# Optimization experiments

Hardware: AMD Instinct MI355X
Metric: run time of the kernel (lower is better)

The kernel has to match this reference:

```python
import jax, jax.numpy as jnp
import numpy as np
import math

K_DIM = 1024
HEADS = 16

def setup_inputs() -> dict:
    key = jax.random.key(0)
    ks = jax.random.split(key, 6)
    b, N, k = 4, 2048, K_DIM
    sc = 1.0 / math.sqrt(k)
    return {
        "x": jax.random.normal(ks[0], (b, N, k), dtype=jnp.float32),
        "Wk": jax.random.normal(ks[1], (k, k), dtype=jnp.float32) * sc,
        "Wq": jax.random.normal(ks[2], (k, k), dtype=jnp.float32) * sc,
        "Wv": jax.random.normal(ks[3], (k, k), dtype=jnp.float32) * sc,
        "Wu": jax.random.normal(ks[4], (k, k), dtype=jnp.float32) * sc,
        "bu": jax.random.normal(ks[5], (k,), dtype=jnp.float32) * 0.01,
    }

def reference(x, Wk, Wq, Wv, Wu, bu):
    b, N, k = x.shape
    h = HEADS
    s = k // h
    # torch Linear: y = x @ W^T
    Q = (x @ Wq.T).reshape(b, N, h, s).transpose(0, 2, 1, 3)  # [b,h,N,s]
    Kh = (x @ Wk.T).reshape(b, N, h, s).transpose(0, 2, 1, 3)
    V = (x @ Wv.T).reshape(b, N, h, s).transpose(0, 2, 1, 3)
    scores = jnp.einsum('bhid,bhjd->bhij', Q, Kh) / math.sqrt(s)  # [b,h,N,N]
    attn = jax.nn.softmax(scores, axis=-1)
    out = jnp.einsum('bhij,bhjd->bhid', attn, V)  # [b,h,N,s]
    out = out.transpose(0, 2, 1, 3).reshape(b, N, k)
    return out @ Wu.T + bu
```

## Files before the change

### kernel.cpp

```cpp
#include <hip/hip_runtime.h>

typedef __bf16 bf16;
typedef __bf16 bf16x4 __attribute__((ext_vector_type(4)));
typedef __bf16 bf16x8 __attribute__((ext_vector_type(8)));
typedef float  f32x4  __attribute__((ext_vector_type(4)));

#define MFMA16(a, b, c) __builtin_amdgcn_mfma_f32_16x16x32_bf16((a), (b), (c), 0, 0, 0)

__device__ __forceinline__ void async_copy16(const void* g, void* l) {
  __builtin_amdgcn_global_load_lds(
      (const __attribute__((address_space(1))) unsigned int*)g,
      (__attribute__((address_space(3))) unsigned int*)l, 16, 0, 0);
}

struct CvtArgs {
  const float* src[5];
  bf16* dst[5];
  int blk_start[6];
};
__global__ void k_cvt_all(CvtArgs a) {
  int b = blockIdx.x;
  int seg = 0;
#pragma unroll
  for (int s = 1; s < 5; ++s) seg += (b >= a.blk_start[s]);
  int i = (b - a.blk_start[seg]) * 2048 + threadIdx.x * 8;
  float4 v0 = *(const float4*)(a.src[seg] + i);
  float4 v1 = *(const float4*)(a.src[seg] + i + 4);
  bf16x8 o = { (bf16)v0.x, (bf16)v0.y, (bf16)v0.z, (bf16)v0.w,
               (bf16)v1.x, (bf16)v1.y, (bf16)v1.z, (bf16)v1.w };
  *(bf16x8*)(a.dst[seg] + i) = o;
}

template <int OUTF32>
__device__ __forceinline__ void gemm128_body(
    const bf16* __restrict__ A, const bf16* __restrict__ B, void* __restrict__ Cp,
    const float* __restrict__ bias, int m0, int n0, int N, int K) {
  __shared__ alignas(16) bf16 As[2][128 * 32];
  __shared__ alignas(16) bf16 Bs[2][128 * 32];
  const int tid = threadIdx.x;
  const int lane = tid & 63;
  const int w = tid >> 6;
  const int quad = lane >> 4;
  const int l16 = lane & 15;
  const int wr = (w >> 1) * 64;
  const int wc = (w & 1) * 64;

  const int srow = tid >> 2;
  const int skk = (tid & 3) * 8;
  const bf16* Ag = A + (long)(m0 + srow) * K + skk;
  const bf16* Bg = B + (long)(n0 + srow) * K + skk;
  const long half = 64L * K;
  bf16* AsW0 = As[0] + w * 512;
  bf16* BsW0 = Bs[0] + w * 512;
  bf16* AsW1 = As[1] + w * 512;
  bf16* BsW1 = Bs[1] + w * 512;

  f32x4 acc[4][4];
#pragma unroll
  for (int i = 0; i < 4; ++i)
#pragma unroll
    for (int j = 0; j < 4; ++j) acc[i][j] = (f32x4){0.f, 0.f, 0.f, 0.f};

  for (int k0 = 0; k0 < K; k0 += 64) {
    async_copy16(Ag + k0, AsW0);
    async_copy16(Ag + half + k0, AsW0 + 2048);
    async_copy16(Bg + k0, BsW0);
    async_copy16(Bg + half + k0, BsW0 + 2048);
    async_copy16(Ag + k0 + 32, AsW1);
    async_copy16(Ag + half + k0 + 32, AsW1 + 2048);
    async_copy16(Bg + k0 + 32, BsW1);
    async_copy16(Bg + half + k0 + 32, BsW1 + 2048);
    __syncthreads();
#pragma unroll
    for (int p = 0; p < 2; ++p) {
      const bf16* AsP = As[p];
      const bf16* BsP = Bs[p];
      bf16x8 af[4], bfr[4];
#pragma unroll
      for (int i = 0; i < 4; ++i)
        af[i] = *(const bf16x8*)&AsP[(wr + i * 16 + l16) * 32 + quad * 8];
#pragma unroll
      for (int j = 0; j < 4; ++j)
        bfr[j] = *(const bf16x8*)&BsP[(wc + j * 16 + l16) * 32 + quad * 8];
#pragma unroll
      for (int i = 0; i < 4; ++i)
#pragma unroll
        for (int j = 0; j < 4; ++j) acc[i][j] = MFMA16(af[i], bfr[j], acc[i][j]);
    }
    __syncthreads();
  }

#pragma unroll
  for (int i = 0; i < 4; ++i)
#pragma unroll
    for (int j = 0; j < 4; ++j)
#pragma unroll
      for (int r = 0; r < 4; ++r) {
        long row = m0 + wr + i * 16 + quad * 4 + r;
        int col = n0 + wc + j * 16 + l16;
        if (OUTF32)
          ((float*)Cp)[row * N + col] = acc[i][j][r] + bias[col];
        else
          ((bf16*)Cp)[row * N + col] = (bf16)acc[i][j][r];
      }
}

#define VMCNT(n) asm volatile("s_waitcnt vmcnt(" #n ")" ::: "memory")
#define SBAR()   asm volatile("s_barrier" ::: "memory")

__device__ __forceinline__ void rdA8(bf16x8 a[4][2], const bf16* S, int base, int c0) {
#pragma unroll
  for (int f = 0; f < 4; ++f) {
    a[f][0] = *(const bf16x8*)(S + base + f * 2048 + c0);
    a[f][1] = *(const bf16x8*)(S + base + f * 2048 + (c0 ^ 32));
  }
}
__device__ __forceinline__ void rdB4(bf16x8 b[2][2], const bf16* S, int base, int c0) {
#pragma unroll
  for (int f = 0; f < 2; ++f) {
    b[f][0] = *(const bf16x8*)(S + base + f * 4096 + c0);
    b[f][1] = *(const bf16x8*)(S + base + f * 4096 + (c0 ^ 32));
  }
}
__device__ __forceinline__ void stg(const bf16* g, bf16* d) {
  async_copy16(g, d);
  async_copy16(g + 64 * 1024, d + 4096);
}

#define MQ(qa, qb)                                             \
  do {                                                         \
    __builtin_amdgcn_s_setprio(1);                             \
    _Pragma("unroll") for (int fa = 0; fa < 4; ++fa)           \
      _Pragma("unroll") for (int fb = 0; fb < 2; ++fb) {       \
        f32x4& cc = acc[(qa) * 4 + fa][(qb) * 2 + fb];         \
        cc = MFMA16(a[fa][0], b[fb][0], cc);                   \
        cc = MFMA16(a[fa][1], b[fb][1], cc);                   \
      }                                                        \
    __builtin_amdgcn_s_setprio(0);                             \
  } while (0)

__global__ __launch_bounds__(512, 2) void k_gemm_qkv256(
    const bf16* __restrict__ xb, const bf16* __restrict__ Wqk, bf16* __restrict__ QKb,
    const bf16* __restrict__ Wvb, bf16* __restrict__ VtG) {
  __shared__ alignas(16) bf16 sm[2 * 4 * 8192];

  const int bid = blockIdx.x;
  const bf16 *A, *B;
  bf16* C;
  int m0, n0, N;
  if (bid < 256) {
    A = xb; B = Wqk; C = QKb;
    m0 = (bid & 31) * 256; n0 = (bid >> 5) * 256; N = 2048;
  } else {
    int id = bid - 256;
    A = Wvb; B = xb; C = VtG;
    m0 = (id >> 5) * 256; n0 = (id & 31) * 256; N = 8192;
  }
  const int tid = threadIdx.x;
  const int lane = tid & 63;
  const int w = tid >> 6;
  const int wm = w >> 2;
  const int wn = w & 3;
  const int quad = lane >> 4;
  const int l16 = lane & 15;

  const int srl = lane >> 3;
  const int scol = ((lane & 7) * 8) ^ (srl << 3);
  const bf16* Ag = A + (long)(m0 + w * 8 + srl) * 1024 + scol;
  const bf16* Bg = B + (long)(n0 + w * 8 + srl) * 1024 + scol;
  const int dl = w * 512;

  const int abase = (wm * 16 + l16) * 64;
  const int bbase = (wn * 16 + l16) * 64;
  const int c0 = (quad * 8) ^ ((l16 & 7) << 3);

  f32x4 acc[8][4];
#pragma unroll
  for (int i = 0; i < 8; ++i)
#pragma unroll
    for (int j = 0; j < 4; ++j) acc[i][j] = (f32x4){0.f, 0.f, 0.f, 0.f};

  stg(Ag, sm + dl);
  stg(Bg, sm + 16384 + dl);
  stg(Bg + 131072, sm + 24576 + dl);
  stg(Ag + 131072, sm + 8192 + dl);
  VMCNT(4);
  SBAR();

  bf16x8 a[4][2], b[2][2];
  for (int t = 0; t < 16; ++t) {
    const bf16* S = sm + (t & 1) * 32768;
    bf16* D = (bf16*)sm + ((t + 1) & 1) * 32768;
    const long ko = (long)((t < 15) ? t + 1 : 15) * 64;

    rdA8(a, S, abase, c0);
    rdB4(b, S + 16384, bbase, c0);
    stg(Ag + ko, D + dl);
    SBAR();
    MQ(0, 0);
    VMCNT(4);
    SBAR();

    rdB4(b, S + 24576, bbase, c0);
    stg(Bg + ko, D + 16384 + dl);
    SBAR();
    MQ(0, 1);
    VMCNT(4);
    SBAR();

    rdA8(a, S + 8192, abase, c0);
    stg(Bg + 131072 + ko, D + 24576 + dl);
    SBAR();
    MQ(1, 1);
    SBAR();

    rdB4(b, S + 16384, bbase, c0);
    stg(Ag + 131072 + ko, D + 8192 + dl);
    SBAR();
    MQ(1, 0);
    VMCNT(4);
    SBAR();
  }

#pragma unroll
  for (int mi = 0; mi < 8; ++mi) {
    long row = m0 + (mi * 2 + wm) * 16 + quad * 4;
#pragma unroll
    for (int ni = 0; ni < 4; ++ni) {
      int col = n0 + (ni * 4 + wn) * 16 + l16;
#pragma unroll
      for (int r = 0; r < 4; ++r)
        C[(row + r) * (long)N + col] = (bf16)acc[mi][ni][r];
    }
  }
  VMCNT(0);
}

__global__ __launch_bounds__(256, 4) void k_gemm_out(
    const bf16* __restrict__ Ab, const bf16* __restrict__ Wub, float* __restrict__ out,
    const float* __restrict__ bu) {
  gemm128_body<1>(Ab, Wub, out, bu, blockIdx.x * 128, blockIdx.y * 128, 1024, 1024);
}

__global__ __launch_bounds__(256, 2) void k_attn(
    const bf16* __restrict__ Q, const bf16* __restrict__ Kb,
    const bf16* __restrict__ Vt, bf16* __restrict__ O) {
  __shared__ alignas(16) bf16 Ps[256][72];
  __shared__ alignas(16) bf16 Ks[64][72];
  __shared__ alignas(16) bf16 Vs[64][72];

  const int tid = threadIdx.x;
  const int lane = tid & 63;
  const int w = tid >> 6;
  const int quad = lane >> 4;
  const int l16 = lane & 15;
  const int bh = blockIdx.x;
  const int qt = blockIdx.y;
  const int bb = bh >> 4;
  const int h = bh & 15;
  const int hoff = h * 64;
  const long rowQ0 = (long)bb * 2048 + qt * 256;
  const long kv0 = (long)bb * 2048;

  {
    const bf16* p = Q + (rowQ0 + tid) * 2048 + hoff;
#pragma unroll
    for (int u = 0; u < 8; ++u) {
      bf16x8 v = *(const bf16x8*)(p + u * 8);
      bf16x8 o;
#pragma unroll
      for (int j = 0; j < 8; ++j) o[j] = (bf16)((float)v[j] * 0.125f);
      *(bf16x8*)&Ps[tid][u * 8] = o;
    }
  }
  bf16x8 bq[4][2];
#pragma unroll
  for (int g = 0; g < 4; ++g)
#pragma unroll
    for (int ss = 0; ss < 2; ++ss)
      bq[g][ss] = *(const bf16x8*)&Ps[w * 64 + g * 16 + l16][ss * 32 + quad * 8];

  f32x4 accO[4][4];
  float lp[4] = {0.f, 0.f, 0.f, 0.f};
#pragma unroll
  for (int g = 0; g < 4; ++g)
#pragma unroll
    for (int t = 0; t < 4; ++t) accO[g][t] = (f32x4){0.f, 0.f, 0.f, 0.f};

  const int srow = tid >> 2;
  const int scol = (tid & 3) * 8;
  const bf16* kp = Kb + (kv0 + srow) * 2048 + hoff + scol;
  const bf16* vp = Vt + (long)(hoff + srow) * 8192 + kv0 + scol;

  bf16x8 kr0 = *(const bf16x8*)kp;
  bf16x8 kr1 = *(const bf16x8*)(kp + 32);
  bf16x8 vr0 = *(const bf16x8*)vp;
  bf16x8 vr1 = *(const bf16x8*)(vp + 32);

  for (int kt = 0; kt < 32; ++kt) {
    __syncthreads();
    *(bf16x8*)&Ks[srow][scol] = kr0;
    *(bf16x8*)&Ks[srow][scol + 32] = kr1;
    *(bf16x8*)&Vs[srow][scol] = vr0;
    *(bf16x8*)&Vs[srow][scol + 32] = vr1;
    __syncthreads();
    if (kt < 31) {
      const bf16* kp2 = kp + (long)(kt + 1) * 64 * 2048;
      const bf16* vp2 = vp + (kt + 1) * 64;
      kr0 = *(const bf16x8*)kp2;
      kr1 = *(const bf16x8*)(kp2 + 32);
      vr0 = *(const bf16x8*)vp2;
      vr1 = *(const bf16x8*)(vp2 + 32);
    }

    bf16x8 ak[4][2], bv[2][4];
#pragma unroll
    for (int mt = 0; mt < 4; ++mt) {
      ak[mt][0] = *(const bf16x8*)&Ks[mt * 16 + l16][quad * 8];
      ak[mt][1] = *(const bf16x8*)&Ks[mt * 16 + l16][32 + quad * 8];
    }
#pragma unroll
    for (int ss = 0; ss < 2; ++ss)
#pragma unroll
      for (int t = 0; t < 4; ++t)
        bv[ss][t] = *(const bf16x8*)&Vs[t * 16 + l16][ss * 32 + quad * 8];

#pragma unroll
    for (int g = 0; g < 4; ++g) {
      f32x4 st[4];
#pragma unroll
      for (int mt = 0; mt < 4; ++mt) {
        st[mt] = (f32x4){0.f, 0.f, 0.f, 0.f};
        st[mt] = MFMA16(ak[mt][0], bq[g][0], st[mt]);
        st[mt] = MFMA16(ak[mt][1], bq[g][1], st[mt]);
      }
#pragma unroll
      for (int mt = 0; mt < 4; ++mt) {
        bf16x4 pk;
#pragma unroll
        for (int r = 0; r < 4; ++r) {
          float pv = __expf(st[mt][r]);
          lp[g] += pv;
          pk[r] = (bf16)pv;
        }
        *(bf16x4*)&Ps[w * 64 + g * 16 + l16][mt * 16 + quad * 4] = pk;
      }
#pragma unroll
      for (int ss = 0; ss < 2; ++ss) {
        bf16x8 ap = *(const bf16x8*)&Ps[w * 64 + g * 16 + l16][ss * 32 + quad * 8];
#pragma unroll
        for (int t = 0; t < 4; ++t)
          accO[g][t] = MFMA16(ap, bv[ss][t], accO[g][t]);
      }
    }
  }

#pragma unroll
  for (int g = 0; g < 4; ++g) {
    float l = lp[g];
    l += __shfl_xor(l, 16);
    l += __shfl_xor(l, 32);
    float linv = 1.f / l;
#pragma unroll
    for (int r = 0; r < 4; ++r) {
      float inv = __shfl(linv, (lane & 48) | (quad * 4 + r));
      long row = rowQ0 + w * 64 + g * 16 + quad * 4 + r;
#pragma unroll
      for (int t = 0; t < 4; ++t)
        O[row * 1024 + hoff + t * 16 + l16] = (bf16)(accO[g][t][r] * inv);
    }
  }
}

extern "C" void kernel_launch(void* const* d_in, const int* in_sizes, int n_in,
                              void* d_out, int out_size, void* d_ws, size_t ws_size,
                              hipStream_t stream) {
  const float* x  = (const float*)d_in[0];
  const float* Wk = (const float*)d_in[1];
  const float* Wq = (const float*)d_in[2];
  const float* Wv = (const float*)d_in[3];
  const float* Wu = (const float*)d_in[4];
  const float* bu = (const float*)d_in[5];
  float* out = (float*)d_out;

  const int XE = 4 * 2048 * 1024;
  const int WE = 1024 * 1024;

  bf16* p = (bf16*)d_ws;
  bf16* xb   = p; p += XE;
  bf16* Wqkb = p; p += 2 * WE;
  bf16* Wvb  = p; p += WE;
  bf16* Wub  = p; p += WE;
  bf16* QKb  = p; p += 2 * XE;
  bf16* VtG  = p; p += XE;
  bf16* Ab   = p; p += XE;

  CvtArgs ca;
  ca.src[0] = x;  ca.dst[0] = xb;
  ca.src[1] = Wq; ca.dst[1] = Wqkb;
  ca.src[2] = Wk; ca.dst[2] = Wqkb + WE;
  ca.src[3] = Wv; ca.dst[3] = Wvb;
  ca.src[4] = Wu; ca.dst[4] = Wub;
  ca.blk_start[0] = 0;
  ca.blk_start[1] = XE / 2048;
  ca.blk_start[2] = ca.blk_start[1] + WE / 2048;
  ca.blk_start[3] = ca.blk_start[2] + WE / 2048;
  ca.blk_start[4] = ca.blk_start[3] + WE / 2048;
  ca.blk_start[5] = ca.blk_start[4] + WE / 2048;
  k_cvt_all<<<ca.blk_start[5], 256, 0, stream>>>(ca);

  k_gemm_qkv256<<<384, 512, 0, stream>>>(xb, Wqkb, QKb, Wvb, VtG);

  k_attn<<<dim3(64, 8), 256, 0, stream>>>(QKb, QKb + 1024, VtG, Ab);

  k_gemm_out<<<dim3(64, 8), 256, 0, stream>>>(Ab, Wub, out, bu);
}
```

Baseline: 260.2 us.

## Revert QKV GEMM to 128-tile body; keep attention P in registers

Replaces the hand-scheduled 256x256 QKV GEMM, with its async LDS pipeline, by the generic 128x128 gemm128_body over a 1536-block grid. In the attention kernel, the exponentiated scores are packed straight into MFMA A-operand registers instead of being written to and re-read from the Ps shared buffer. V is stored into shared memory with its k-index positions permuted so that it lines up with the register layout of P. The register path removes an LDS round trip per tile, while the GEMM swap gives up the deeper pipelined large-tile schedule.

Result: faster. 252.8 us (-2.9%).

```diff
diff --git a/kernel.cpp b/kernel.cpp
--- a/kernel.cpp
+++ b/kernel.cpp
@@ -105,135 +105,22 @@
       }
 }
 
-#define VMCNT(n) asm volatile("s_waitcnt vmcnt(" #n ")" ::: "memory")
-#define SBAR()   asm volatile("s_barrier" ::: "memory")
-
-__device__ __forceinline__ void rdA8(bf16x8 a[4][2], const bf16* S, int base, int c0) {
-#pragma unroll
-  for (int f = 0; f < 4; ++f) {
-    a[f][0] = *(const bf16x8*)(S + base + f * 2048 + c0);
-    a[f][1] = *(const bf16x8*)(S + base + f * 2048 + (c0 ^ 32));
-  }
-}
-__device__ __forceinline__ void rdB4(bf16x8 b[2][2], const bf16* S, int base, int c0) {
-#pragma unroll
-  for (int f = 0; f < 2; ++f) {
-    b[f][0] = *(const bf16x8*)(S + base + f * 4096 + c0);
-    b[f][1] = *(const bf16x8*)(S + base + f * 4096 + (c0 ^ 32));
-  }
-}
-__device__ __forceinline__ void stg(const bf16* g, bf16* d) {
-  async_copy16(g, d);
-  async_copy16(g + 64 * 1024, d + 4096);
-}
-
-#define MQ(qa, qb)                                             \
-  do {                                                         \
-    __builtin_amdgcn_s_setprio(1);                             \
-    _Pragma("unroll") for (int fa = 0; fa < 4; ++fa)           \
-      _Pragma("unroll") for (int fb = 0; fb < 2; ++fb) {       \
-        f32x4& cc = acc[(qa) * 4 + fa][(qb) * 2 + fb];         \
-        cc = MFMA16(a[fa][0], b[fb][0], cc);                   \
-        cc = MFMA16(a[fa][1], b[fb][1], cc);                   \
-      }                                                        \
-    __builtin_amdgcn_s_setprio(0);                             \
-  } while (0)
-
-__global__ __launch_bounds__(512, 2) void k_gemm_qkv256(
+__global__ __launch_bounds__(256, 4) void k_gemm_qkv(
     const bf16* __restrict__ xb, const bf16* __restrict__ Wqk, bf16* __restrict__ QKb,
     const bf16* __restrict__ Wvb, bf16* __restrict__ VtG) {
-  __shared__ alignas(16) bf16 sm[2 * 4 * 8192];
-
-  const int bid = blockIdx.x;
+  int bid = blockIdx.x;
   const bf16 *A, *B;
   bf16* C;
   int m0, n0, N;
-  if (bid < 256) {
+  if (bid < 1024) {
     A = xb; B = Wqk; C = QKb;
-    m0 = (bid & 31) * 256; n0 = (bid >> 5) * 256; N = 2048;
+    m0 = (bid & 63) * 128; n0 = (bid >> 6) * 128; N = 2048;
   } else {
-    int id = bid - 256;
+    int id = bid - 1024;
     A = Wvb; B = xb; C = VtG;
-    m0 = (id >> 5) * 256; n0 = (id & 31) * 256; N = 8192;
-  }
-  const int tid = threadIdx.x;
-  const int lane = tid & 63;
-  const int w = tid >> 6;
-  const int wm = w >> 2;
-  const int wn = w & 3;
-  const int quad = lane >> 4;
-  const int l16 = lane & 15;
-
-  const int srl = lane >> 3;
-  const int scol = ((lane & 7) * 8) ^ (srl << 3);
-  const bf16* Ag = A + (long)(m0 + w * 8 + srl) * 1024 + scol;
-  const bf16* Bg = B + (long)(n0 + w * 8 + srl) * 1024 + scol;
-  const int dl = w * 512;
-
-  const int abase = (wm * 16 + l16) * 64;
-  const int bbase = (wn * 16 + l16) * 64;
-  const int c0 = (quad * 8) ^ ((l16 & 7) << 3);
-
-  f32x4 acc[8][4];
-#pragma unroll
-  for (int i = 0; i < 8; ++i)
-#pragma unroll
-    for (int j = 0; j < 4; ++j) acc[i][j] = (f32x4){0.f, 0.f, 0.f, 0.f};
-
-  stg(Ag, sm + dl);
-  stg(Bg, sm + 16384 + dl);
-  stg(Bg + 131072, sm + 24576 + dl);
-  stg(Ag + 131072, sm + 8192 + dl);
-  VMCNT(4);
-  SBAR();
-
-  bf16x8 a[4][2], b[2][2];
-  for (int t = 0; t < 16; ++t) {
-    const bf16* S = sm + (t & 1) * 32768;
-    bf16* D = (bf16*)sm + ((t + 1) & 1) * 32768;
-    const long ko = (long)((t < 15) ? t + 1 : 15) * 64;
-
-    rdA8(a, S, abase, c0);
-    rdB4(b, S + 16384, bbase, c0);
-    stg(Ag + ko, D + dl);
-    SBAR();
-    MQ(0, 0);
-    VMCNT(4);
-    SBAR();
-
-    rdB4(b, S + 24576, bbase, c0);
-    stg(Bg + ko, D + 16384 + dl);
-    SBAR();
-    MQ(0, 1);
-    VMCNT(4);
-    SBAR();
-
-    rdA8(a, S + 8192, abase, c0);
-    stg(Bg + 131072 + ko, D + 24576 + dl);
-    SBAR();
-    MQ(1, 1);
-    SBAR();
-
-    rdB4(b, S + 16384, bbase, c0);
-    stg(Ag + 131072 + ko, D + 8192 + dl);
-    SBAR();
-    MQ(1, 0);
-    VMCNT(4);
-    SBAR();
-  }
-
-#pragma unroll
-  for (int mi = 0; mi < 8; ++mi) {
-    long row = m0 + (mi * 2 + wm) * 16 + quad * 4;
-#pragma unroll
-    for (int ni = 0; ni < 4; ++ni) {
-      int col = n0 + (ni * 4 + wn) * 16 + l16;
-#pragma unroll
-      for (int r = 0; r < 4; ++r)
-        C[(row + r) * (long)N + col] = (bf16)acc[mi][ni][r];
-    }
-  }
-  VMCNT(0);
+    m0 = (id >> 6) * 128; n0 = (id & 63) * 128; N = 8192;
+  }
+  gemm128_body<0>(A, B, C, nullptr, m0, n0, N, 1024);
 }
 
 __global__ __launch_bounds__(256, 4) void k_gemm_out(
@@ -289,6 +176,7 @@
 
   const int srow = tid >> 2;
   const int scol = (tid & 3) * 8;
+  const int c0p = ((scol & 8) << 1) | ((scol & 16) >> 2);
   const bf16* kp = Kb + (kv0 + srow) * 2048 + hoff + scol;
   const bf16* vp = Vt + (long)(hoff + srow) * 8192 + kv0 + scol;
 
@@ -301,8 +189,16 @@
     __syncthreads();
     *(bf16x8*)&Ks[srow][scol] = kr0;
     *(bf16x8*)&Ks[srow][scol + 32] = kr1;
-    *(bf16x8*)&Vs[srow][scol] = vr0;
-    *(bf16x8*)&Vs[srow][scol + 32] = vr1;
+    {
+      bf16x4 lo0 = {vr0[0], vr0[1], vr0[2], vr0[3]};
+      bf16x4 hi0 = {vr0[4], vr0[5], vr0[6], vr0[7]};
+      bf16x4 lo1 = {vr1[0], vr1[1], vr1[2], vr1[3]};
+      bf16x4 hi1 = {vr1[4], vr1[5], vr1[6], vr1[7]};
+      *(bf16x4*)&Vs[srow][c0p] = lo0;
+      *(bf16x4*)&Vs[srow][c0p + 8] = hi0;
+      *(bf16x4*)&Vs[srow][c0p + 32] = lo1;
+      *(bf16x4*)&Vs[srow][c0p + 40] = hi1;
+    }
     __syncthreads();
     if (kt < 31) {
       const bf16* kp2 = kp + (long)(kt + 1) * 64 * 2048;
@@ -334,24 +230,21 @@
         st[mt] = MFMA16(ak[mt][0], bq[g][0], st[mt]);
         st[mt] = MFMA16(ak[mt][1], bq[g][1], st[mt]);
       }
+      bf16x8 apf[2];
 #pragma unroll
       for (int mt = 0; mt < 4; ++mt) {
-        bf16x4 pk;
 #pragma unroll
         for (int r = 0; r < 4; ++r) {
           float pv = __expf(st[mt][r]);
           lp[g] += pv;
-          pk[r] = (bf16)pv;
+          apf[mt >> 1][(mt & 1) * 4 + r] = (bf16)pv;
         }
-        *(bf16x4*)&Ps[w * 64 + g * 16 + l16][mt * 16 + quad * 4] = pk;
       }
 #pragma unroll
-      for (int ss = 0; ss < 2; ++ss) {
-        bf16x8 ap = *(const bf16x8*)&Ps[w * 64 + g * 16 + l16][ss * 32 + quad * 8];
+      for (int ss = 0; ss < 2; ++ss)
 #pragma unroll
         for (int t = 0; t < 4; ++t)
-          accO[g][t] = MFMA16(ap, bv[ss][t], accO[g][t]);
-      }
+          accO[g][t] = MFMA16(apf[ss], bv[ss][t], accO[g][t]);
     }
   }
 
@@ -409,7 +302,7 @@
   ca.blk_start[5] = ca.blk_start[4] + WE / 2048;
   k_cvt_all<<<ca.blk_start[5], 256, 0, stream>>>(ca);
 
-  k_gemm_qkv256<<<384, 512, 0, stream>>>(xb, Wqkb, QKb, Wvb, VtG);
+  k_gemm_qkv<<<1536, 256, 0, stream>>>(xb, Wqkb, QKb, Wvb, VtG);
 
   k_attn<<<dim3(64, 8), 256, 0, stream>>>(QKb, QKb + 1024, VtG, Ab);
 
```
